# Performance work log

Measured on AMD Instinct MI355X. Metric: run time of the kernel, lower is better.

## Reference

```python
import jax, jax.numpy as jnp
import numpy as np

N, T, HIDDEN = 32768, 2048, 128
NF = T // 2 + 1  # rfft bins


def setup_inputs() -> dict:
    key = jax.random.key(0)
    k1, k2, kw1, kw2 = jax.random.split(key, 4)
    x1 = jax.random.normal(k1, (N, T), dtype=jnp.float32)
    x2 = jax.random.normal(k2, (N, T), dtype=jnp.float32)
    # kaiming_uniform (relu): bound = sqrt(6 / fan_in)
    fan1 = 2 * NF
    W1 = jax.random.uniform(kw1, (HIDDEN, fan1), minval=-np.sqrt(6.0 / fan1), maxval=np.sqrt(6.0 / fan1), dtype=jnp.float32)
    b1 = jnp.zeros((HIDDEN,), dtype=jnp.float32)
    W2 = jax.random.uniform(kw2, (T, HIDDEN), minval=-np.sqrt(6.0 / HIDDEN), maxval=np.sqrt(6.0 / HIDDEN), dtype=jnp.float32)
    b2 = jnp.zeros((T,), dtype=jnp.float32)
    return {"x1": x1, "x2": x2, "W1": W1, "b1": b1, "W2": W2, "b2": b2}


def reference(x1, x2, W1, b1, W2, b2):
    # batched rfft replaces the per-sample Python loop
    diff = jnp.fft.rfft(x1, axis=-1) - jnp.fft.rfft(x2, axis=-1)  # [N, NF] complex
    feats = jnp.concatenate([diff.real, diff.imag], axis=-1)       # [N, 2*NF]
    h = jax.nn.relu(feats @ W1.T + b1)                             # [N, HIDDEN]
    out = h @ W2.T + b2                                            # [N, T]
    return jnp.mean(out, axis=-1)                                  # [N]
```

## Files before the change

kernel.cpp:

```cpp
#include <hip/hip_runtime.h>
#include <hip/hip_bf16.h>
#include <math.h>

#define T_LEN   2048
#define NFREQ   1025
#define HID     128
#define NSAMP   32768
#define NIT     64

typedef __attribute__((ext_vector_type(8)))  short short8v;
typedef __attribute__((ext_vector_type(16))) float f32x16;

#define AKG_OFF    0
#define W2BAR_OFF  (1u<<20)
#define B2BAR_OFF  ((1u<<20)+512)
#define PW_OFF     ((1u<<20)+1024)
#define PB_OFF     ((1u<<20)+1024+8192)

__global__ __launch_bounds__(128) void k_w2_partial(const float* __restrict__ W2,
                                                    const float* __restrict__ b2,
                                                    float* __restrict__ pw,
                                                    float* __restrict__ pb) {
    const int b = blockIdx.x;
    const int c = threadIdx.x;
    const int t0 = b * 128;
    float s0 = 0.f, s1 = 0.f, s2 = 0.f, s3 = 0.f;
    #pragma unroll 4
    for (int i = 0; i < 128; i += 4) {
        s0 += W2[(long)(t0 + i + 0) * HID + c];
        s1 += W2[(long)(t0 + i + 1) * HID + c];
        s2 += W2[(long)(t0 + i + 2) * HID + c];
        s3 += W2[(long)(t0 + i + 3) * HID + c];
    }
    pw[b * HID + c] = (s0 + s1) + (s2 + s3);
    float v = b2[t0 + c];
    for (int o = 32; o > 0; o >>= 1) v += __shfl_down(v, o);
    __shared__ float sred[2];
    if ((threadIdx.x & 63) == 0) sred[threadIdx.x >> 6] = v;
    __syncthreads();
    if (threadIdx.x == 0) pb[b] = sred[0] + sred[1];
}

__global__ __launch_bounds__(128) void k_w2_final(const float* __restrict__ pw,
                                                  const float* __restrict__ pb,
                                                  float* __restrict__ w2bar,
                                                  float* __restrict__ b2bar) {
    const int c = threadIdx.x;
    float s = 0.f;
    #pragma unroll
    for (int b = 0; b < 16; ++b) s += pw[b * HID + c];
    w2bar[c] = s * (1.f / (float)T_LEN);
    if (c == 0) {
        float t = 0.f;
        #pragma unroll
        for (int b = 0; b < 16; ++b) t += pb[b];
        *b2bar = t * (1.f / (float)T_LEN);
    }
}

__global__ __launch_bounds__(256) void k_build_At(const float* __restrict__ W1,
                                                  unsigned short* __restrict__ Akg) {
    __shared__ float lW[2 * NFREQ];
    const int k  = blockIdx.x >> 4;
    const int tg = blockIdx.x & 15;
    const int tid = threadIdx.x;
    const float* __restrict__ Wk = W1 + (long)k * (2 * NFREQ);
    for (int i = tid; i < 2 * NFREQ; i += 256) lW[i] = Wk[i];
    __syncthreads();
    const float* __restrict__ lWr = lW;
    const float* __restrict__ lWi = lW + NFREQ;

    const int chunk = tid >> 6;
    const int fh = (tid >> 5) & 1;
    const int tl = tid & 31;
    const int t  = tg * 128 + chunk * 32 + tl;

    const float w = -6.283185307179586f / (float)T_LEN;
    float sr, cr;
    { int ph2 = (2 * t) & (T_LEN - 1); sincosf(w * (float)ph2, &sr, &cr); }
    float zr, zi;
    { int ph = (t * fh) & (T_LEN - 1); sincosf(w * (float)ph, &zi, &zr); }
    float acc = 0.f;
    int f = fh;
    for (int blk = 0; blk < 4; ++blk) {
        #pragma unroll 4
        for (int j = 0; j < 128; ++j) {
            acc = fmaf(lWr[f], zr, acc);
            acc = fmaf(lWi[f], zi, acc);
            float nzr = fmaf(zr, cr, -(zi * sr));
            float nzi = fmaf(zr, sr, zi * cr);
            zr = nzr; zi = nzi;
            f += 2;
        }
        int ph = (t * f) & (T_LEN - 1);
        sincosf(w * (float)ph, &zi, &zr);
    }
    if (fh == 0) {
        acc = fmaf(lWr[1024], zr, acc);
        acc = fmaf(lWi[1024], zi, acc);
    }
    acc += __shfl_xor(acc, 32);

    if (fh == 0) {
        __hip_bfloat16 hb = __float2bfloat16(acc);
        float hf = __bfloat162float(hb);
        __hip_bfloat16 lb = __float2bfloat16(acc - hf);
        const int tile = t >> 5, islot = (t & 31) >> 3, j = t & 7;
        const int shi = islot ^ (k & 7);
        const int slo = (islot ^ 4) ^ (k & 7);
        const long base = (long)tile * 8192 + k * 64 + j;
        Akg[base + shi * 8] = __builtin_bit_cast(unsigned short, hb);
        Akg[base + slo * 8] = __builtin_bit_cast(unsigned short, lb);
    }
}

__global__ __launch_bounds__(512) void k_gemm(const float* __restrict__ x1,
                                              const float* __restrict__ x2,
                                              const unsigned short* __restrict__ Akg,
                                              const float* __restrict__ b1,
                                              const float* __restrict__ w2bar,
                                              const float* __restrict__ b2bar,
                                              float* __restrict__ out) {
    __shared__ __align__(16) unsigned short ak[2][8192];
    __shared__ __align__(16) unsigned short dd[2][8192];
    __shared__ float osum[128];

    const int tid = threadIdx.x;
    const int l   = tid & 63;
    const int w   = tid >> 6;
    const int wm  = w & 3;
    const int wn  = w >> 2;
    const int g   = l >> 5;
    const int m31 = l & 31;
    const long row0 = (long)blockIdx.x * 128;

    const int rs = tid >> 2;
    const int j4 = tid & 3;
    const float* __restrict__ px1 = x1 + (row0 + rs) * T_LEN + j4 * 8;
    const float* __restrict__ px2 = x2 + (row0 + rs) * T_LEN + j4 * 8;
    const unsigned short* __restrict__ pak = Akg + tid * 16;

    const int wr_hi = rs * 64 + ((j4 ^ (rs & 7)) * 8);
    const int ra  = wm * 32 + m31;
    const int rb0 = wn * 64 + m31;
    const int rb1 = wn * 64 + 32 + m31;

    f32x16 acc[2];
    #pragma unroll
    for (int tj = 0; tj < 2; ++tj)
        #pragma unroll
        for (int q = 0; q < 16; ++q) acc[tj][q] = 0.f;

    float4 xa0, xa1, xb0, xb1;
    uint4  akr0, akr1;
    xa0 = *(const float4*)(px1);     xa1 = *(const float4*)(px1 + 4);
    xb0 = *(const float4*)(px2);     xb1 = *(const float4*)(px2 + 4);
    akr0 = *(const uint4*)(pak);     akr1 = *(const uint4*)(pak + 8);

    for (int it = 0; it < NIT; ++it) {
        const int buf = it & 1;
        float dv[8] = {xa0.x - xb0.x, xa0.y - xb0.y, xa0.z - xb0.z, xa0.w - xb0.w,
                       xa1.x - xb1.x, xa1.y - xb1.y, xa1.z - xb1.z, xa1.w - xb1.w};
        short8v dhv, dlv;
        #pragma unroll
        for (int e = 0; e < 8; ++e) {
            __hip_bfloat16 hb = __float2bfloat16(dv[e]);
            float lo = dv[e] - __bfloat162float(hb);
            dhv[e] = __builtin_bit_cast(short, hb);
            dlv[e] = __builtin_bit_cast(short, __float2bfloat16(lo));
        }
        *(short8v*)&dd[buf][wr_hi]      = dhv;
        *(short8v*)&dd[buf][wr_hi ^ 32] = dlv;
        *(uint4*)&ak[buf][tid * 16]     = akr0;
        *(uint4*)&ak[buf][tid * 16 + 8] = akr1;

        if (it + 1 < NIT) {
            const float* p1 = px1 + (it + 1) * 32;
            const float* p2 = px2 + (it + 1) * 32;
            xa0 = *(const float4*)(p1);     xa1 = *(const float4*)(p1 + 4);
            xb0 = *(const float4*)(p2);     xb1 = *(const float4*)(p2 + 4);
            const unsigned short* pa = pak + (long)(it + 1) * 8192;
            akr0 = *(const uint4*)(pa);     akr1 = *(const uint4*)(pa + 8);
        }

        __syncthreads();

        #pragma unroll
        for (int kc = 0; kc < 2; ++kc) {
            const int sa = ((2 * kc + g) ^ (ra & 7)) * 8;
            const short8v ah = *(const short8v*)&dd[buf][ra * 64 + sa];
            const short8v al = *(const short8v*)&dd[buf][ra * 64 + (sa ^ 32)];
            #pragma unroll
            for (int tj = 0; tj < 2; ++tj) {
                const int r = (tj == 0) ? rb0 : rb1;
                const int sb = ((2 * kc + g) ^ (r & 7)) * 8;
                const short8v bh = *(const short8v*)&ak[buf][r * 64 + sb];
                const short8v bl = *(const short8v*)&ak[buf][r * 64 + (sb ^ 32)];
                acc[tj] = __builtin_amdgcn_mfma_f32_32x32x16_bf16(ah, bh, acc[tj], 0, 0, 0);
                acc[tj] = __builtin_amdgcn_mfma_f32_32x32x16_bf16(ah, bl, acc[tj], 0, 0, 0);
                acc[tj] = __builtin_amdgcn_mfma_f32_32x32x16_bf16(al, bh, acc[tj], 0, 0, 0);
            }
        }
    }

    float pres[16];
    #pragma unroll
    for (int q = 0; q < 16; ++q) pres[q] = 0.f;
    #pragma unroll
    for (int tj = 0; tj < 2; ++tj) {
        const int n = wn * 64 + tj * 32 + m31;
        const float bb1 = b1[n], wb = w2bar[n];
        #pragma unroll
        for (int q = 0; q < 16; ++q)
            pres[q] += fmaxf(acc[tj][q] + bb1, 0.f) * wb;
    }
    #pragma unroll
    for (int q = 0; q < 16; ++q) {
        float s = pres[q];
        s += __shfl_xor(s, 1); s += __shfl_xor(s, 2); s += __shfl_xor(s, 4);
        s += __shfl_xor(s, 8); s += __shfl_xor(s, 16);
        pres[q] = s;
    }
    __syncthreads();
    if (wn == 0 && m31 == 0) {
        #pragma unroll
        for (int q = 0; q < 16; ++q)
            osum[wm * 32 + (q & 3) + 8 * (q >> 2) + 4 * g] = pres[q];
    }
    __syncthreads();
    if (wn == 1 && m31 == 0) {
        const float bb = *b2bar;
        #pragma unroll
        for (int q = 0; q < 16; ++q) {
            const int m = wm * 32 + (q & 3) + 8 * (q >> 2) + 4 * g;
            out[row0 + m] = pres[q] + osum[m] + bb;
        }
    }
}

extern "C" void kernel_launch(void* const* d_in, const int* in_sizes, int n_in,
                              void* d_out, int out_size, void* d_ws, size_t ws_size,
                              hipStream_t stream) {
    const float* x1 = (const float*)d_in[0];
    const float* x2 = (const float*)d_in[1];
    const float* W1 = (const float*)d_in[2];
    const float* b1 = (const float*)d_in[3];
    const float* W2 = (const float*)d_in[4];
    const float* b2 = (const float*)d_in[5];
    float* out = (float*)d_out;

    char* ws = (char*)d_ws;
    unsigned short* Akg = (unsigned short*)(ws + AKG_OFF);
    float* w2bar = (float*)(ws + W2BAR_OFF);
    float* b2bar = (float*)(ws + B2BAR_OFF);
    float* pw    = (float*)(ws + PW_OFF);
    float* pb    = (float*)(ws + PB_OFF);

    hipLaunchKernelGGL(k_w2_partial, dim3(16), dim3(128), 0, stream, W2, b2, pw, pb);
    hipLaunchKernelGGL(k_w2_final,   dim3(1),  dim3(128), 0, stream, pw, pb, w2bar, b2bar);
    hipLaunchKernelGGL(k_build_At,   dim3(2048), dim3(256), 0, stream, W1, Akg);
    hipLaunchKernelGGL(k_gemm,       dim3(NSAMP / 128), dim3(512), 0, stream,
                       x1, x2, Akg, b1, w2bar, b2bar, out);
}
```

Measured before the change: 566.8 us.

## Deepen global prefetch to two stages with LDS-only barrier in main loop

Unrolls the K loop by two and keeps two register sets of prefetched x1/x2/Akg tiles, so global loads are issued two iterations ahead instead of one. It replaces __syncthreads with a barrier that waits only on LDS counters (lgkmcnt), so outstanding global loads need not drain at the barrier. The aim is to hide global-memory latency in this streaming, memory-bound kernel. In exchange it uses more registers, which may lower occupancy, and it issues redundant clamped loads on the final iterations.

```diff
diff --git a/kernel.cpp b/kernel.cpp
--- a/kernel.cpp
+++ b/kernel.cpp
@@ -145,74 +145,96 @@
     const int rb0 = wn * 64 + m31;
     const int rb1 = wn * 64 + 32 + m31;
 
-    f32x16 acc[2];
-    #pragma unroll
-    for (int tj = 0; tj < 2; ++tj)
-        #pragma unroll
-        for (int q = 0; q < 16; ++q) acc[tj][q] = 0.f;
-
-    float4 xa0, xa1, xb0, xb1;
-    uint4  akr0, akr1;
-    xa0 = *(const float4*)(px1);     xa1 = *(const float4*)(px1 + 4);
-    xb0 = *(const float4*)(px2);     xb1 = *(const float4*)(px2 + 4);
-    akr0 = *(const uint4*)(pak);     akr1 = *(const uint4*)(pak + 8);
-
-    for (int it = 0; it < NIT; ++it) {
-        const int buf = it & 1;
-        float dv[8] = {xa0.x - xb0.x, xa0.y - xb0.y, xa0.z - xb0.z, xa0.w - xb0.w,
-                       xa1.x - xb1.x, xa1.y - xb1.y, xa1.z - xb1.z, xa1.w - xb1.w};
-        short8v dhv, dlv;
-        #pragma unroll
-        for (int e = 0; e < 8; ++e) {
-            __hip_bfloat16 hb = __float2bfloat16(dv[e]);
-            float lo = dv[e] - __bfloat162float(hb);
-            dhv[e] = __builtin_bit_cast(short, hb);
-            dlv[e] = __builtin_bit_cast(short, __float2bfloat16(lo));
+    f32x16 acc0, acc1;
+    #pragma unroll
+    for (int q = 0; q < 16; ++q) { acc0[q] = 0.f; acc1[q] = 0.f; }
+
+    float4 xa0A, xa1A, xb0A, xb1A, xa0B, xa1B, xb0B, xb1B;
+    uint4  ak0A, ak1A, ak0B, ak1B;
+
+#define LOADX(S, IT) {                                                      \
+        const float* p1_ = px1 + (IT) * 32;                                 \
+        const float* p2_ = px2 + (IT) * 32;                                 \
+        xa0##S = *(const float4*)(p1_);  xa1##S = *(const float4*)(p1_ + 4);\
+        xb0##S = *(const float4*)(p2_);  xb1##S = *(const float4*)(p2_ + 4);\
+        const unsigned short* pa_ = pak + (long)(IT) * 8192;                \
+        ak0##S = *(const uint4*)(pa_);   ak1##S = *(const uint4*)(pa_ + 8); }
+
+#define STAGE(S, BUF) {                                                     \
+        float dv_[8] = {xa0##S.x - xb0##S.x, xa0##S.y - xb0##S.y,           \
+                        xa0##S.z - xb0##S.z, xa0##S.w - xb0##S.w,           \
+                        xa1##S.x - xb1##S.x, xa1##S.y - xb1##S.y,           \
+                        xa1##S.z - xb1##S.z, xa1##S.w - xb1##S.w};          \
+        short8v dhv_, dlv_;                                                 \
+        _Pragma("unroll")                                                   \
+        for (int e = 0; e < 8; ++e) {                                       \
+            __hip_bfloat16 hb_ = __float2bfloat16(dv_[e]);                  \
+            float lo_ = dv_[e] - __bfloat162float(hb_);                     \
+            dhv_[e] = __builtin_bit_cast(short, hb_);                       \
+            dlv_[e] = __builtin_bit_cast(short, __float2bfloat16(lo_));     \
+        }                                                                   \
+        *(short8v*)&dd[BUF][wr_hi]      = dhv_;                             \
+        *(short8v*)&dd[BUF][wr_hi ^ 32] = dlv_;                             \
+        *(uint4*)&ak[BUF][tid * 16]     = ak0##S;                           \
+        *(uint4*)&ak[BUF][tid * 16 + 8] = ak1##S; }
+
+#define LBAR() { asm volatile("s_waitcnt lgkmcnt(0)" ::: "memory");         \
+                 __builtin_amdgcn_s_barrier();                              \
+                 __builtin_amdgcn_sched_barrier(0); }
+
+#define COMPUTE2(BUF, ACCA, ACCB) {                                         \
+        _Pragma("unroll")                                                   \
+        for (int kc = 0; kc < 2; ++kc) {                                    \
+            const int sa_ = ((2 * kc + g) ^ (ra & 7)) * 8;                  \
+            const short8v ah_ = *(const short8v*)&dd[BUF][ra * 64 + sa_];   \
+            const short8v al_ = *(const short8v*)&dd[BUF][ra * 64 + (sa_ ^ 32)]; \
+            const int sb0_ = ((2 * kc + g) ^ (rb0 & 7)) * 8;                \
+            const short8v bh0_ = *(const short8v*)&ak[BUF][rb0 * 64 + sb0_];\
+            const short8v bl0_ = *(const short8v*)&ak[BUF][rb0 * 64 + (sb0_ ^ 32)]; \
+            const int sb1_ = ((2 * kc + g) ^ (rb1 & 7)) * 8;                \
+            const short8v bh1_ = *(const short8v*)&ak[BUF][rb1 * 64 + sb1_];\
+            const short8v bl1_ = *(const short8v*)&ak[BUF][rb1 * 64 + (sb1_ ^ 32)]; \
+            ACCA = __builtin_amdgcn_mfma_f32_32x32x16_bf16(ah_, bh0_, ACCA, 0, 0, 0); \
+            ACCA = __builtin_amdgcn_mfma_f32_32x32x16_bf16(ah_, bl0_, ACCA, 0, 0, 0); \
+            ACCA = __builtin_amdgcn_mfma_f32_32x32x16_bf16(al_, bh0_, ACCA, 0, 0, 0); \
+            ACCB = __builtin_amdgcn_mfma_f32_32x32x16_bf16(ah_, bh1_, ACCB, 0, 0, 0); \
+            ACCB = __builtin_amdgcn_mfma_f32_32x32x16_bf16(ah_, bl1_, ACCB, 0, 0, 0); \
+            ACCB = __builtin_amdgcn_mfma_f32_32x32x16_bf16(al_, bh1_, ACCB, 0, 0, 0); \
+        } }
+
+    LOADX(A, 0);
+    LOADX(B, 1);
+
+    for (int it2 = 0; it2 < NIT / 2; ++it2) {
+        const int itA = 2 * it2;
+        STAGE(A, 0);
+        { int itn = itA + 2; if (itn > NIT - 1) itn = NIT - 1; LOADX(A, itn); }
+        LBAR();
+        COMPUTE2(0, acc0, acc1);
+        STAGE(B, 1);
+        { int itn = itA + 3; if (itn > NIT - 1) itn = NIT - 1; LOADX(B, itn); }
+        LBAR();
+        COMPUTE2(1, acc0, acc1);
+    }
+
+#undef LOADX
+#undef STAGE
+#undef LBAR
+#undef COMPUTE2
+
+    float pres[16];
+    #pragma unroll
+    for (int q = 0; q < 16; ++q) pres[q] = 0.f;
+    {
+        const int n0 = wn * 64 + m31;
+        const float bb0 = b1[n0], wb0 = w2bar[n0];
+        const int n1 = wn * 64 + 32 + m31;
+        const float bb1v = b1[n1], wb1 = w2bar[n1];
+        #pragma unroll
+        for (int q = 0; q < 16; ++q) {
+            pres[q] += fmaxf(acc0[q] + bb0, 0.f) * wb0;
+            pres[q] += fmaxf(acc1[q] + bb1v, 0.f) * wb1;
         }
-        *(short8v*)&dd[buf][wr_hi]      = dhv;
-        *(short8v*)&dd[buf][wr_hi ^ 32] = dlv;
-        *(uint4*)&ak[buf][tid * 16]     = akr0;
-        *(uint4*)&ak[buf][tid * 16 + 8] = akr1;
-
-        if (it + 1 < NIT) {
-            const float* p1 = px1 + (it + 1) * 32;
-            const float* p2 = px2 + (it + 1) * 32;
-            xa0 = *(const float4*)(p1);     xa1 = *(const float4*)(p1 + 4);
-            xb0 = *(const float4*)(p2);     xb1 = *(const float4*)(p2 + 4);
-            const unsigned short* pa = pak + (long)(it + 1) * 8192;
-            akr0 = *(const uint4*)(pa);     akr1 = *(const uint4*)(pa + 8);
-        }
-
-        __syncthreads();
-
-        #pragma unroll
-        for (int kc = 0; kc < 2; ++kc) {
-            const int sa = ((2 * kc + g) ^ (ra & 7)) * 8;
-            const short8v ah = *(const short8v*)&dd[buf][ra * 64 + sa];
-            const short8v al = *(const short8v*)&dd[buf][ra * 64 + (sa ^ 32)];
-            #pragma unroll
-            for (int tj = 0; tj < 2; ++tj) {
-                const int r = (tj == 0) ? rb0 : rb1;
-                const int sb = ((2 * kc + g) ^ (r & 7)) * 8;
-                const short8v bh = *(const short8v*)&ak[buf][r * 64 + sb];
-                const short8v bl = *(const short8v*)&ak[buf][r * 64 + (sb ^ 32)];
-                acc[tj] = __builtin_amdgcn_mfma_f32_32x32x16_bf16(ah, bh, acc[tj], 0, 0, 0);
-                acc[tj] = __builtin_amdgcn_mfma_f32_32x32x16_bf16(ah, bl, acc[tj], 0, 0, 0);
-                acc[tj] = __builtin_amdgcn_mfma_f32_32x32x16_bf16(al, bh, acc[tj], 0, 0, 0);
-            }
-        }
-    }
-
-    float pres[16];
-    #pragma unroll
-    for (int q = 0; q < 16; ++q) pres[q] = 0.f;
-    #pragma unroll
-    for (int tj = 0; tj < 2; ++tj) {
-        const int n = wn * 64 + tj * 32 + m31;
-        const float bb1 = b1[n], wb = w2bar[n];
-        #pragma unroll
-        for (int q = 0; q < 16; ++q)
-            pres[q] += fmaxf(acc[tj][q] + bb1, 0.f) * wb;
     }
     #pragma unroll
     for (int q = 0; q < 16; ++q) {
```

Result: slower. 598.5 us (+5.6%).
